# Kernel tuning notes

Measured on AMD Instinct MI355X. Metric: run time of the kernel, lower is better.

The kernel has to match this reference:

```python
import jax, jax.numpy as jnp
import numpy as np

B, S, D, H = 4, 2048, 1024, 16
HD = D // H  # head_dim = 64


def setup_inputs() -> dict:
    key = jax.random.key(0)
    ks = jax.random.split(key, 5)
    s = 1.0 / np.sqrt(D)
    return {
        "x": jax.random.normal(ks[0], (B, S, D), jnp.float32),
        "Wq": jax.random.normal(ks[1], (D, D), jnp.float32) * s,
        "Wk": jax.random.normal(ks[2], (D, D), jnp.float32) * s,
        "Wv": jax.random.normal(ks[3], (D, D), jnp.float32) * s,
        "Wo": jax.random.normal(ks[4], (D, D), jnp.float32) * s,
        "bo": jnp.zeros((D,), jnp.float32),
    }


def reference(x, Wq, Wk, Wv, Wo, bo):
    b, s, d = x.shape
    # projections (torch Linear: x @ W.T; weights here stored as [in, out] equivalent)
    q = (x @ Wq).reshape(b, s, H, HD).transpose(0, 2, 1, 3)  # [b,h,s,hd]
    k = (x @ Wk).reshape(b, s, H, HD).transpose(0, 2, 1, 3)
    v = (x @ Wv).reshape(b, s, H, HD).transpose(0, 2, 1, 3)
    scores = jnp.einsum("bhqd,bhkd->bhqk", q, k) * (HD ** -0.5)
    causal = jnp.tril(jnp.ones((s, s), bool))  # mask==0 -> -inf
    scores = jnp.where(causal, scores, -jnp.inf)
    attn = jax.nn.softmax(scores, axis=-1)
    out = jnp.einsum("bhqk,bhkd->bhqd", attn, v)
    out = out.transpose(0, 2, 1, 3).reshape(b, s, d)
    return out @ Wo + bo
```

## Files before the change

### kernel.cpp

```cpp
#include <hip/hip_runtime.h>
#include <cstdint>
#include <cstddef>

typedef __attribute__((ext_vector_type(8))) short bf16x8;
typedef __attribute__((ext_vector_type(4))) short bf16x4;
typedef __attribute__((ext_vector_type(4))) float f32x4;

constexpr int Bsz = 4, Ssz = 2048, Dsz = 1024, Hn = 16, HDsz = 64;
constexpr int Msz = Bsz * Ssz;
constexpr float LOG2E = 1.4426950408889634f;

#define MFMA16(a, b, c) __builtin_amdgcn_mfma_f32_16x16x16bf16_1k(a, b, c, 0, 0, 0)
#define MFMA32(a, b, c) __builtin_amdgcn_mfma_f32_16x16x32_bf16(a, b, c, 0, 0, 0)

__device__ __forceinline__ unsigned short f2bf(float f) {
  union { float f; unsigned int u; } v; v.f = f;
  unsigned int r = v.u + 0x7fffu + ((v.u >> 16) & 1u);
  return (unsigned short)(r >> 16);
}

typedef __attribute__((address_space(1))) const unsigned int gu32;
typedef __attribute__((address_space(3))) unsigned int lu32;
__device__ __forceinline__ void async_cp16(const unsigned short* g, unsigned short* l) {
  __builtin_amdgcn_global_load_lds((gu32*)g, (lu32*)l, 16, 0, 0);
}

__global__ void prep_kernel(const float* __restrict__ x, unsigned short* __restrict__ xb,
                            const float* __restrict__ W0, const float* __restrict__ W1,
                            const float* __restrict__ W2, const float* __restrict__ W3,
                            unsigned short* __restrict__ T0, unsigned short* __restrict__ T1,
                            unsigned short* __restrict__ T2, unsigned short* __restrict__ T3) {
  const int z = blockIdx.z;
  if (z == 4) {
    const int i0 = (blockIdx.y * 32 + blockIdx.x) * 2048 + threadIdx.x;
#pragma unroll
    for (int j = 0; j < 8; j++) {
      const int i = i0 + j * 256;
      const float4 v = reinterpret_cast<const float4*>(x)[i];
      ushort4 o;
      o.x = f2bf(v.x); o.y = f2bf(v.y); o.z = f2bf(v.z); o.w = f2bf(v.w);
      reinterpret_cast<ushort4*>(xb)[i] = o;
    }
    return;
  }
  __shared__ float tile[32][33];
  const float* W = (z == 0) ? W0 : (z == 1) ? W1 : (z == 2) ? W2 : W3;
  unsigned short* Wt = (z == 0) ? T0 : (z == 1) ? T1 : (z == 2) ? T2 : T3;
  int tx = threadIdx.x & 31, ty = threadIdx.x >> 5;
  int bx = blockIdx.x, by = blockIdx.y;
#pragma unroll
  for (int i = 0; i < 4; i++) {
    int k = by * 32 + ty + i * 8;
    tile[ty + i * 8][tx] = W[k * Dsz + bx * 32 + tx];
  }
  __syncthreads();
#pragma unroll
  for (int i = 0; i < 4; i++) {
    int nrow = bx * 32 + ty + i * 8;
    Wt[nrow * Dsz + by * 32 + tx] = f2bf(tile[tx][ty + i * 8]);
  }
}

enum { EPI_QKV = 0, EPI_OUT = 1 };

template <int EPI>
__global__ __launch_bounds__(512, 4)
void gemm_bk64(const unsigned short* __restrict__ A,
               const unsigned short* __restrict__ Bt,
               unsigned short* __restrict__ Qh,
               unsigned short* __restrict__ Kh,
               unsigned short* __restrict__ Vth,
               float* __restrict__ Out,
               const float* __restrict__ bias) {
  __shared__ unsigned short As[128 * 64];
  __shared__ unsigned short Bs[128 * 64];

  const int tid = threadIdx.x;
  const int w = tid >> 6, lane = tid & 63;
  const int l15 = lane & 15, quad = lane >> 4;
  const int wr = w >> 1, wc = w & 1;
  const int orig = blockIdx.y * gridDim.x + blockIdx.x;
  const int xcd = orig & 7, idx = orig >> 3;
  const int bm = (xcd << 3) | (idx & 7);
  const int bn = idx >> 3;
  const int rr = lane >> 3;
  const int scoff = ((lane & 7) ^ rr) * 8;

  f32x4 acc[2][4];
#pragma unroll
  for (int i = 0; i < 2; i++)
#pragma unroll
    for (int j = 0; j < 4; j++) acc[i][j] = (f32x4){0.f, 0.f, 0.f, 0.f};

  const int rowA0 = bm * 128, rowB0 = bn * 128;

  for (int kt = 0; kt < Dsz / 64; kt++) {
#pragma unroll
    for (int i = 0; i < 2; i++) {
      const int r8 = w * 16 + i * 8;
      async_cp16(&A[(size_t)(rowA0 + r8 + rr) * Dsz + kt * 64 + scoff], &As[r8 * 64]);
      async_cp16(&Bt[(size_t)(rowB0 + r8 + rr) * Dsz + kt * 64 + scoff], &Bs[r8 * 64]);
    }
    __syncthreads();

#pragma unroll
    for (int ks = 0; ks < 2; ks++) {
      bf16x8 af[2], bfr[4];
#pragma unroll
      for (int t = 0; t < 2; t++) {
        const int ra = wr * 32 + t * 16 + l15;
        af[t] = *reinterpret_cast<const bf16x8*>(
            &As[ra * 64 + (((ks * 4 + quad) ^ (ra & 7)) * 8)]);
      }
#pragma unroll
      for (int t = 0; t < 4; t++) {
        const int rb = wc * 64 + t * 16 + l15;
        bfr[t] = *reinterpret_cast<const bf16x8*>(
            &Bs[rb * 64 + (((ks * 4 + quad) ^ (rb & 7)) * 8)]);
      }
#pragma unroll
      for (int i = 0; i < 2; i++)
#pragma unroll
        for (int j = 0; j < 4; j++)
          acc[i][j] = MFMA32(af[i], bfr[j], acc[i][j]);
    }
    __syncthreads();
  }

  if (EPI == EPI_QKV) {
    const int proj = (bn * 128) >> 10;
#pragma unroll
    for (int i = 0; i < 2; i++) {
#pragma unroll
      for (int j = 0; j < 4; j++) {
        const int n = bn * 128 + wc * 64 + j * 16 + l15;
        const int nn = n & 1023, h = nn >> 6, hd = nn & 63;
        const int m0 = bm * 128 + wr * 32 + i * 16 + quad * 4;
        const int b = m0 >> 11, s0 = m0 & (Ssz - 1);
        if (proj == 0) {
#pragma unroll
          for (int r = 0; r < 4; r++)
            Qh[((size_t)(b * Hn + h) * Ssz + s0 + r) * HDsz + hd] =
                f2bf(acc[i][j][r] * (0.125f * LOG2E));
        } else if (proj == 1) {
#pragma unroll
          for (int r = 0; r < 4; r++)
            Kh[((size_t)(b * Hn + h) * Ssz + s0 + r) * HDsz + hd] = f2bf(acc[i][j][r]);
        } else {
          ushort4 o;
          o.x = f2bf(acc[i][j][0]); o.y = f2bf(acc[i][j][1]);
          o.z = f2bf(acc[i][j][2]); o.w = f2bf(acc[i][j][3]);
          *reinterpret_cast<ushort4*>(
              &Vth[((size_t)(b * Hn + h) * HDsz + hd) * Ssz + s0]) = o;
        }
      }
    }
  } else {
#pragma unroll
    for (int i = 0; i < 2; i++) {
#pragma unroll
      for (int j = 0; j < 4; j++) {
        const int n = bn * 128 + wc * 64 + j * 16 + l15;
        const int m0 = bm * 128 + wr * 32 + i * 16 + quad * 4;
#pragma unroll
        for (int r = 0; r < 4; r++)
          Out[(size_t)(m0 + r) * Dsz + n] = acc[i][j][r] + bias[n];
      }
    }
  }
}

__global__ __launch_bounds__(256, 8)
void flash_kernel(const unsigned short* __restrict__ Q,
                  const unsigned short* __restrict__ Kg,
                  const unsigned short* __restrict__ Vt,
                  unsigned short* __restrict__ AO) {
  __shared__ unsigned short Ks[64 * 64];
  __shared__ unsigned short Vs[64 * 64];

  const int tid = threadIdx.x;
  const int w = tid >> 6, lane = tid & 63;
  const int l15 = lane & 15, quad = lane >> 4;
  const int rr = lane >> 3;

  const int linear = blockIdx.y * 16 + blockIdx.x;
  const int bh = (linear & 7) * 8 + ((linear >> 3) & 7);
  const int g = linear >> 6;
  const int gk = g >> 2, gr = g & 3;
  const int t = (gk < 4) ? (gr * 8 + gk) : (31 - (gr * 8 + (gk - 4)));

  const unsigned short* Qb = Q + (size_t)bh * Ssz * HDsz;
  const unsigned short* Kb = Kg + (size_t)bh * Ssz * HDsz;
  const unsigned short* Vb = Vt + (size_t)bh * HDsz * Ssz;
  const int b = bh / Hn, h = bh % Hn;

  const int hl = (l15 & 7) ^ ((l15 >> 3) << 2);

  const int q0 = t * 64;
  const int rowStart = q0 + w * 16;

  bf16x8 qf[2];
#pragma unroll
  for (int ks = 0; ks < 2; ks++)
    qf[ks] = *reinterpret_cast<const bf16x8*>(
        &Qb[(size_t)(rowStart + l15) * HDsz + ks * 32 + quad * 8]);

  f32x4 oacc[4];
  float lpart = 0.f;
#pragma unroll
  for (int to = 0; to < 4; to++) oacc[to] = (f32x4){0.f, 0.f, 0.f, 0.f};

  const int nkb = t + 1;
  for (int kb = 0; kb < nkb; kb++) {
    const int kv0 = kb * 64;
#pragma unroll
    for (int i = 0; i < 2; i++) {
      const int r8 = w * 16 + i * 8;
      const int sc = (((lane & 7) ^ rr ^ (i << 2))) * 8;
      async_cp16(&Kb[(size_t)(kv0 + r8 + rr) * HDsz + sc], &Ks[r8 * 64]);
      async_cp16(&Vb[(size_t)(r8 + rr) * Ssz + kv0 + sc], &Vs[r8 * 64]);
    }
    __syncthreads();

    f32x4 sc[4];
#pragma unroll
    for (int tn = 0; tn < 4; tn++) sc[tn] = (f32x4){0.f, 0.f, 0.f, 0.f};
#pragma unroll
    for (int ks = 0; ks < 2; ks++) {
#pragma unroll
      for (int tn = 0; tn < 4; tn++) {
        const int rk = tn * 16 + l15;
        bf16x8 kf = *reinterpret_cast<const bf16x8*>(
            &Ks[rk * 64 + (((ks * 4 + quad) ^ hl) * 8)]);
        sc[tn] = MFMA32(kf, qf[ks], sc[tn]);
      }
    }

    const bool needMask = (kv0 + 63 > rowStart);
    if (needMask) {
      const int qrow = rowStart + l15;
#pragma unroll
      for (int tn = 0; tn < 4; tn++)
#pragma unroll
        for (int r = 0; r < 4; r++)
          if (kv0 + tn * 16 + quad * 4 + r > qrow) sc[tn][r] = -1e30f;
    }

    unsigned int pk[4][2];
#pragma unroll
    for (int tn = 0; tn < 4; tn++) {
      union { float f; unsigned int u; } e0, e1, e2, e3;
      e0.f = __builtin_amdgcn_exp2f(sc[tn][0]);
      e1.f = __builtin_amdgcn_exp2f(sc[tn][1]);
      e2.f = __builtin_amdgcn_exp2f(sc[tn][2]);
      e3.f = __builtin_amdgcn_exp2f(sc[tn][3]);
      lpart += (e0.f + e1.f) + (e2.f + e3.f);
      pk[tn][0] = __builtin_amdgcn_perm(e1.u, e0.u, 0x07060302u);
      pk[tn][1] = __builtin_amdgcn_perm(e3.u, e2.u, 0x07060302u);
    }

#pragma unroll
    for (int tn = 0; tn < 4; tn++) {
      union { unsigned int u[2]; bf16x4 v; } cv;
      cv.u[0] = pk[tn][0]; cv.u[1] = pk[tn][1];
      const bf16x4 pa = cv.v;
#pragma unroll
      for (int to = 0; to < 4; to++) {
        const int rv = to * 16 + l15;
        const int chunk = tn * 2 + (quad >> 1);
        bf16x4 vf = *reinterpret_cast<const bf16x4*>(
            (const char*)Vs + rv * 128 + ((chunk ^ hl) * 16) + (quad & 1) * 8);
        oacc[to] = MFMA16(pa, vf, oacc[to]);
      }
    }
    __syncthreads();
  }

  float lf = lpart;
  lf += __shfl_xor(lf, 16);
  lf += __shfl_xor(lf, 32);
  float linv[4];
#pragma unroll
  for (int r = 0; r < 4; r++) {
    union { float f; int i; } cv;
    cv.f = lf;
    cv.i = __builtin_amdgcn_ds_bpermute((quad * 4 + r) * 4, cv.i);
    linv[r] = 1.f / cv.f;
  }
#pragma unroll
  for (int r = 0; r < 4; r++) {
    const int s = rowStart + quad * 4 + r;
    const size_t m = (size_t)b * Ssz + s;
#pragma unroll
    for (int to = 0; to < 4; to++) {
      const int n = h * HDsz + to * 16 + l15;
      AO[m * Dsz + n] = f2bf(oacc[to][r] * linv[r]);
    }
  }
}

extern "C" void kernel_launch(void* const* d_in, const int* in_sizes, int n_in,
                              void* d_out, int out_size, void* d_ws, size_t ws_size,
                              hipStream_t stream) {
  const float* x  = (const float*)d_in[0];
  const float* Wq = (const float*)d_in[1];
  const float* Wk = (const float*)d_in[2];
  const float* Wv = (const float*)d_in[3];
  const float* Wo = (const float*)d_in[4];
  const float* bo = (const float*)d_in[5];
  float* out = (float*)d_out;

  unsigned short* xb  = (unsigned short*)d_ws;
  unsigned short* Wqt = xb + (size_t)Msz * Dsz;
  unsigned short* Wkt = Wqt + (size_t)Dsz * Dsz;
  unsigned short* Wvt = Wkt + (size_t)Dsz * Dsz;
  unsigned short* Wot = Wvt + (size_t)Dsz * Dsz;
  unsigned short* Qh  = Wot + (size_t)Dsz * Dsz;
  unsigned short* Kh  = Qh + (size_t)Msz * Dsz;
  unsigned short* Vth = Kh + (size_t)Msz * Dsz;
  unsigned short* AO  = Vth + (size_t)Msz * Dsz;

  prep_kernel<<<dim3(32, 32, 5), 256, 0, stream>>>(
      x, xb, Wq, Wk, Wv, Wo, Wqt, Wkt, Wvt, Wot);

  gemm_bk64<EPI_QKV><<<dim3(3 * Dsz / 128, Msz / 128), 512, 0, stream>>>(
      xb, Wqt, Qh, Kh, Vth, nullptr, nullptr);

  flash_kernel<<<dim3(16, 128), 256, 0, stream>>>(Qh, Kh, Vth, AO);

  gemm_bk64<EPI_OUT><<<dim3(Dsz / 128, Msz / 128), 512, 0, stream>>>(
      AO, Wot, nullptr, nullptr, nullptr, out, bo);
}
```

Before: 240.8 us.

## Switch flash attention to 32x32 MFMA tiles with 128-row query blocks

Rewrites the attention inner loop to use 32x32x16 bf16 MFMA for both QK^T and PV, with each wave handling 32 query rows and each block 128 rows. Probabilities are packed with v_cvt_pk_bf16_f32 and v_permlane32_swap so the score layout feeds the PV MFMA directly. Fully masked 32-key sub-tiles are skipped, and the block scheduling order changes. The intent is fewer MFMA issues and LDS reads per FLOP, with more K/V reuse. The costs are more registers, lower occupancy, and half as many blocks.

Measured after the change: 227.3 us. -5.6%, faster.

```diff
diff --git a/kernel.cpp b/kernel.cpp
--- a/kernel.cpp
+++ b/kernel.cpp
@@ -3,20 +3,29 @@
 #include <cstddef>
 
 typedef __attribute__((ext_vector_type(8))) short bf16x8;
-typedef __attribute__((ext_vector_type(4))) short bf16x4;
 typedef __attribute__((ext_vector_type(4))) float f32x4;
+typedef __attribute__((ext_vector_type(16))) float f32x16;
 
 constexpr int Bsz = 4, Ssz = 2048, Dsz = 1024, Hn = 16, HDsz = 64;
 constexpr int Msz = Bsz * Ssz;
 constexpr float LOG2E = 1.4426950408889634f;
 
-#define MFMA16(a, b, c) __builtin_amdgcn_mfma_f32_16x16x16bf16_1k(a, b, c, 0, 0, 0)
 #define MFMA32(a, b, c) __builtin_amdgcn_mfma_f32_16x16x32_bf16(a, b, c, 0, 0, 0)
+#define MFMA3232(a, b, c) __builtin_amdgcn_mfma_f32_32x32x16_bf16(a, b, c, 0, 0, 0)
 
 __device__ __forceinline__ unsigned short f2bf(float f) {
   union { float f; unsigned int u; } v; v.f = f;
   unsigned int r = v.u + 0x7fffu + ((v.u >> 16) & 1u);
   return (unsigned short)(r >> 16);
+}
+
+__device__ __forceinline__ int cvtpk(float a, float b) {
+  int r;
+  asm("v_cvt_pk_bf16_f32 %0, %1, %2" : "=v"(r) : "v"(a), "v"(b));
+  return r;
+}
+__device__ __forceinline__ void pswap(int& a, int& b) {
+  asm("v_permlane32_swap_b32 %0, %1" : "+v"(a), "+v"(b));
 }
 
 typedef __attribute__((address_space(1))) const unsigned int gu32;
@@ -170,7 +179,7 @@
   }
 }
 
-__global__ __launch_bounds__(256, 8)
+__global__ __launch_bounds__(256, 4)
 void flash_kernel(const unsigned short* __restrict__ Q,
                   const unsigned short* __restrict__ Kg,
                   const unsigned short* __restrict__ Vt,
@@ -180,37 +189,38 @@
 
   const int tid = threadIdx.x;
   const int w = tid >> 6, lane = tid & 63;
-  const int l15 = lane & 15, quad = lane >> 4;
+  const int l31 = lane & 31, hi = lane >> 5;
   const int rr = lane >> 3;
 
   const int linear = blockIdx.y * 16 + blockIdx.x;
   const int bh = (linear & 7) * 8 + ((linear >> 3) & 7);
-  const int g = linear >> 6;
-  const int gk = g >> 2, gr = g & 3;
-  const int t = (gk < 4) ? (gr * 8 + gk) : (31 - (gr * 8 + (gk - 4)));
+  const int g = linear >> 6, gk = g >> 2, ga = g & 3;
+  const int t = (gk == 0) ? 15 - ga : (gk == 1) ? 8 + ga : (gk == 2) ? 7 - ga : ga;
 
   const unsigned short* Qb = Q + (size_t)bh * Ssz * HDsz;
   const unsigned short* Kb = Kg + (size_t)bh * Ssz * HDsz;
   const unsigned short* Vb = Vt + (size_t)bh * HDsz * Ssz;
   const int b = bh / Hn, h = bh % Hn;
 
-  const int hl = (l15 & 7) ^ ((l15 >> 3) << 2);
-
-  const int q0 = t * 64;
-  const int rowStart = q0 + w * 16;
-
-  bf16x8 qf[2];
-#pragma unroll
-  for (int ks = 0; ks < 2; ks++)
+  const int hl = (l31 & 7) ^ (((l31 >> 3) & 1) << 2);
+
+  const int rowStart = t * 128 + w * 32;
+  const int q = rowStart + l31;
+
+  bf16x8 qf[4];
+#pragma unroll
+  for (int ks = 0; ks < 4; ks++)
     qf[ks] = *reinterpret_cast<const bf16x8*>(
-        &Qb[(size_t)(rowStart + l15) * HDsz + ks * 32 + quad * 8]);
-
-  f32x4 oacc[4];
+        &Qb[(size_t)q * HDsz + ks * 16 + hi * 8]);
+
+  f32x16 oacc[2];
+#pragma unroll
+  for (int ho = 0; ho < 2; ho++)
+#pragma unroll
+    for (int r = 0; r < 16; r++) oacc[ho][r] = 0.f;
   float lpart = 0.f;
-#pragma unroll
-  for (int to = 0; to < 4; to++) oacc[to] = (f32x4){0.f, 0.f, 0.f, 0.f};
-
-  const int nkb = t + 1;
+
+  const int nkb = 2 * t + 2;
   for (int kb = 0; kb < nkb; kb++) {
     const int kv0 = kb * 64;
 #pragma unroll
@@ -222,79 +232,79 @@
     }
     __syncthreads();
 
-    f32x4 sc[4];
-#pragma unroll
-    for (int tn = 0; tn < 4; tn++) sc[tn] = (f32x4){0.f, 0.f, 0.f, 0.f};
-#pragma unroll
-    for (int ks = 0; ks < 2; ks++) {
-#pragma unroll
-      for (int tn = 0; tn < 4; tn++) {
-        const int rk = tn * 16 + l15;
+#pragma unroll
+    for (int kt = 0; kt < 2; kt++) {
+      const bool skip = (kv0 + kt * 32 >= rowStart + 32);
+      if (skip) continue;
+
+      f32x16 st;
+#pragma unroll
+      for (int r = 0; r < 16; r++) st[r] = 0.f;
+#pragma unroll
+      for (int ks = 0; ks < 4; ks++) {
+        const int row = kt * 32 + l31;
         bf16x8 kf = *reinterpret_cast<const bf16x8*>(
-            &Ks[rk * 64 + (((ks * 4 + quad) ^ hl) * 8)]);
-        sc[tn] = MFMA32(kf, qf[ks], sc[tn]);
-      }
-    }
-
-    const bool needMask = (kv0 + 63 > rowStart);
-    if (needMask) {
-      const int qrow = rowStart + l15;
-#pragma unroll
-      for (int tn = 0; tn < 4; tn++)
-#pragma unroll
-        for (int r = 0; r < 4; r++)
-          if (kv0 + tn * 16 + quad * 4 + r > qrow) sc[tn][r] = -1e30f;
-    }
-
-    unsigned int pk[4][2];
-#pragma unroll
-    for (int tn = 0; tn < 4; tn++) {
-      union { float f; unsigned int u; } e0, e1, e2, e3;
-      e0.f = __builtin_amdgcn_exp2f(sc[tn][0]);
-      e1.f = __builtin_amdgcn_exp2f(sc[tn][1]);
-      e2.f = __builtin_amdgcn_exp2f(sc[tn][2]);
-      e3.f = __builtin_amdgcn_exp2f(sc[tn][3]);
-      lpart += (e0.f + e1.f) + (e2.f + e3.f);
-      pk[tn][0] = __builtin_amdgcn_perm(e1.u, e0.u, 0x07060302u);
-      pk[tn][1] = __builtin_amdgcn_perm(e3.u, e2.u, 0x07060302u);
-    }
-
-#pragma unroll
-    for (int tn = 0; tn < 4; tn++) {
-      union { unsigned int u[2]; bf16x4 v; } cv;
-      cv.u[0] = pk[tn][0]; cv.u[1] = pk[tn][1];
-      const bf16x4 pa = cv.v;
-#pragma unroll
-      for (int to = 0; to < 4; to++) {
-        const int rv = to * 16 + l15;
-        const int chunk = tn * 2 + (quad >> 1);
-        bf16x4 vf = *reinterpret_cast<const bf16x4*>(
-            (const char*)Vs + rv * 128 + ((chunk ^ hl) * 16) + (quad & 1) * 8);
-        oacc[to] = MFMA16(pa, vf, oacc[to]);
+            &Ks[row * 64 + (((ks * 2 + hi) ^ hl) * 8)]);
+        st = MFMA3232(kf, qf[ks], st);
+      }
+
+      const bool needMask = (kv0 + kt * 32 + 31 > rowStart);
+      if (needMask) {
+#pragma unroll
+        for (int r = 0; r < 16; r++) {
+          const int kv = kv0 + kt * 32 + (r & 3) + 8 * (r >> 2) + 4 * hi;
+          if (kv > q) st[r] = -1e30f;
+        }
+      }
+
+      float e[16];
+#pragma unroll
+      for (int r = 0; r < 16; r++) e[r] = __builtin_amdgcn_exp2f(st[r]);
+#pragma unroll
+      for (int r = 0; r < 16; r += 4)
+        lpart += (e[r] + e[r + 1]) + (e[r + 2] + e[r + 3]);
+
+#pragma unroll
+      for (int s = 0; s < 2; s++) {
+        int a0 = cvtpk(e[8 * s + 0], e[8 * s + 1]);
+        int a1 = cvtpk(e[8 * s + 2], e[8 * s + 3]);
+        int b0 = cvtpk(e[8 * s + 4], e[8 * s + 5]);
+        int b1 = cvtpk(e[8 * s + 6], e[8 * s + 7]);
+        pswap(a0, b0);
+        pswap(a1, b1);
+        union { int u[4]; bf16x8 v; } pa;
+        pa.u[0] = a0; pa.u[1] = a1; pa.u[2] = b0; pa.u[3] = b1;
+        const int t16 = kt * 2 + s;
+#pragma unroll
+        for (int ho = 0; ho < 2; ho++) {
+          const int row = ho * 32 + l31;
+          bf16x8 vf = *reinterpret_cast<const bf16x8*>(
+              &Vs[row * 64 + (((t16 * 2 + hi) ^ hl) * 8)]);
+          oacc[ho] = MFMA3232(pa.v, vf, oacc[ho]);
+        }
       }
     }
     __syncthreads();
   }
 
-  float lf = lpart;
-  lf += __shfl_xor(lf, 16);
-  lf += __shfl_xor(lf, 32);
-  float linv[4];
-#pragma unroll
-  for (int r = 0; r < 4; r++) {
+  float lf = lpart + __shfl_xor(lpart, 32);
+  float linv[16];
+#pragma unroll
+  for (int r = 0; r < 16; r++) {
+    const int qloc = (r & 3) + 8 * (r >> 2) + 4 * hi;
     union { float f; int i; } cv;
     cv.f = lf;
-    cv.i = __builtin_amdgcn_ds_bpermute((quad * 4 + r) * 4, cv.i);
+    cv.i = __builtin_amdgcn_ds_bpermute(qloc * 4, cv.i);
     linv[r] = 1.f / cv.f;
   }
 #pragma unroll
-  for (int r = 0; r < 4; r++) {
-    const int s = rowStart + quad * 4 + r;
-    const size_t m = (size_t)b * Ssz + s;
-#pragma unroll
-    for (int to = 0; to < 4; to++) {
-      const int n = h * HDsz + to * 16 + l15;
-      AO[m * Dsz + n] = f2bf(oacc[to][r] * linv[r]);
+  for (int r = 0; r < 16; r++) {
+    const int qloc = (r & 3) + 8 * (r >> 2) + 4 * hi;
+    const size_t m = (size_t)b * Ssz + rowStart + qloc;
+#pragma unroll
+    for (int ho = 0; ho < 2; ho++) {
+      const int n = h * HDsz + ho * 32 + l31;
+      AO[m * Dsz + n] = f2bf(oacc[ho][r] * linv[r]);
     }
   }
 }
@@ -326,7 +336,7 @@
   gemm_bk64<EPI_QKV><<<dim3(3 * Dsz / 128, Msz / 128), 512, 0, stream>>>(
       xb, Wqt, Qh, Kh, Vth, nullptr, nullptr);
 
-  flash_kernel<<<dim3(16, 128), 256, 0, stream>>>(Qh, Kh, Vth, AO);
+  flash_kernel<<<dim3(16, Bsz * Hn), 256, 0, stream>>>(Qh, Kh, Vth, AO);
 
   gemm_bk64<EPI_OUT><<<dim3(Dsz / 128, Msz / 128), 512, 0, stream>>>(
       AO, Wot, nullptr, nullptr, nullptr, out, bo);
```
